# Kernel optimization log

Measured on AMD Instinct MI355X. Metric: run time of the kernel, lower is better.

The kernel has to match this reference:

```python
import jax, jax.numpy as jnp
import numpy as np

# Module / shape constants (match init_kwargs and forward-path constants)
H = 8          # heads
DH = 80        # dim_head
QDIM = 640     # query_dim == inner_dim (context = x, self-attention content branch)
B = 1
NQ = 2048      # query tokens
NS = 2048      # injected style tokens
T = 1.2        # injection_config['T']  (attn_matrix_scale)
GAMMA = 0.3    # injection_config['gamma'] (q_mix)
LAMBDA_MAX = 2.5
TOPK = 128     # style_topk
STYLE_SCALE = 1.0
SCALE = DH ** -0.5


def _split_heads(t, h):
    # 'b n (h d) -> (b h) n d'
    b, n, hd = t.shape
    return t.reshape(b, n, h, hd // h).transpose(0, 2, 1, 3).reshape(b * h, n, hd // h)


def setup_inputs() -> dict:
    key = jax.random.key(0)
    ks = jax.random.split(key, 9)
    x = jax.random.normal(ks[0], (B, NQ, QDIM), jnp.float32)
    Q_c_injected = jax.random.normal(ks[1], (H, NQ, DH), jnp.float32) * 0.5
    K_s_injected = jax.random.normal(ks[2], (H, NS, DH), jnp.float32) * 0.5
    V_s_injected = jax.random.normal(ks[3], (H, NS, DH), jnp.float32) * 0.5
    # Learned params (nn.Linear weights are [out, in]; no bias on q/k/v)
    Wq = jax.random.normal(ks[4], (H * DH, QDIM), jnp.float32) * 0.02
    Wk = jax.random.normal(ks[5], (H * DH, QDIM), jnp.float32) * 0.02
    Wv = jax.random.normal(ks[6], (H * DH, QDIM), jnp.float32) * 0.02
    Wo = jax.random.normal(ks[7], (QDIM, H * DH), jnp.float32) * 0.02
    bo = jnp.zeros((QDIM,), jnp.float32)
    ada_gate = jnp.array([0.2], jnp.float32)
    return {"x": x, "Q_c_injected": Q_c_injected, "K_s_injected": K_s_injected,
            "V_s_injected": V_s_injected, "Wq": Wq, "Wk": Wk, "Wv": Wv,
            "Wo": Wo, "bo": bo, "ada_gate": ada_gate}


def reference(x, Q_c_injected, K_s_injected, V_s_injected, Wq, Wk, Wv, Wo, bo, ada_gate):
    b, n, _ = x.shape
    # Projections, context = x
    q_cs = _split_heads(x @ Wq.T, H)                    # (b h) n d
    k_cs = _split_heads(x @ Wk.T, H)                    # (b h) m d
    v_cs = _split_heads(x @ Wv.T, H)
    Q_c = jnp.tile(Q_c_injected, (b, 1, 1))             # torch.cat([Q_c]*b)
    q = Q_c * GAMMA + q_cs * (1.0 - GAMMA)              # Q_hat_cs
    K_s = jnp.tile(K_s_injected, (b, 1, 1))
    V_s = jnp.tile(V_s_injected, (b, 1, 1))

    style = jnp.einsum('bid,bjd->bij', q, K_s) * (T * SCALE)   # (bh) nq ns
    content = jnp.einsum('bid,bjd->bij', q, k_cs) * SCALE       # (bh) nq nc
    ns = style.shape[-1]
    s4 = style.reshape(b, H, n, ns)
    c4 = content.reshape(b, H, n, -1)

    # Per-head logsumexp gating between style and content branches
    r = jax.scipy.special.logsumexp(s4, axis=-1) - jax.scipy.special.logsumexp(c4, axis=-1)
    r = jnp.clip(r, -20.0, 20.0).mean(axis=1)           # (b, nq)
    lam = 1.0 + (LAMBDA_MAX - 1.0) * jax.nn.sigmoid(r)  # lambda_map
    style = (s4 * lam[:, None, :, None]).reshape(b * H, n, ns)

    # Top-k sparsification of style logits (scatter top-k values onto -inf canvas)
    vals, idx = jax.lax.top_k(style, TOPK)
    neg = jnp.finfo(style.dtype).min
    bi = jnp.arange(b * H)[:, None, None]
    ni = jnp.arange(n)[None, :, None]
    style = jnp.full_like(style, neg).at[bi, ni, idx].set(vals)

    logits = jnp.concatenate([style, content], axis=-1)
    attn = jax.nn.softmax(logits, axis=-1)
    v = jnp.concatenate([V_s * STYLE_SCALE, v_cs], axis=1)      # (bh) (ns+nc) d
    out = jnp.einsum('bij,bjd->bid', attn, v)

    # AdaIN-style modulation
    A = attn.reshape(b, H, n, -1)
    Vh = v.reshape(b, H, -1, DH)
    Qh = q.reshape(b, H, n, DH)
    Vmean = jnp.einsum('bhnm,bhmd->bhnd', A, Vh)
    mu = Qh.mean(axis=2, keepdims=True)
    var = Qh.var(axis=2, keepdims=True)                 # unbiased=False
    Qn = (Qh - mu) / jnp.sqrt(var + 1e-5)
    Vsq = jnp.einsum('bhnm,bhmd->bhnd', A, Vh * Vh)
    Vstd = jnp.sqrt(jnp.clip(Vsq - Vmean ** 2, 1e-5))
    out_mod = (Vstd * Qn + Vmean).reshape(b * H, n, DH)  # use_std_scale path

    g = jnp.tanh(ada_gate[0])                            # use_residual_gate
    out = out + g * (out_mod - out)
    out = out.reshape(b, H, n, DH).transpose(0, 2, 1, 3).reshape(b, n, H * DH)
    return out @ Wo.T + bo                               # to_out (dropout=0)
```

## Files before the change

### kernel.cpp

```cpp
#include <hip/hip_runtime.h>
#include <hip/hip_fp16.h>
#include <math.h>

#define NH 8
#define DH 80
#define NTOK 2048
#define QD 640
#define SCALE_F 0.11180339887498949f
#define TSCALE_F (1.2f * SCALE_F)
#define GAMMA_F 0.3f
#define LMAX_F 2.5f
#define TOPKN 128

typedef __attribute__((ext_vector_type(8))) short bf16x8;
typedef __attribute__((ext_vector_type(4))) float f32x4;
typedef __attribute__((ext_vector_type(4))) unsigned short u16x4;

#define OFF_QB   0u
#define OFF_OB   1310720u
#define OFF_QH   2621440u
#define OFF_QL   3407872u
#define OFF_KCH  4194304u
#define OFF_KSH  4980736u
#define OFF_KSL  5767168u
#define OFF_VCT  6553600u
#define OFF_VCQT 7208960u
#define OFF_VST  7864320u
#define OFF_VSQT 8519680u
#define OFF_OP   9175040u
#define OFF_SP   14417920u
#define OFF_DEN  19660800u
#define OFF_MSZ  19726336u
#define OFF_LSZ  19791872u
#define OFF_MCZ  19857408u
#define OFF_LCZ  19922944u
#define OFF_M    19988480u
#define OFF_LAM  20004864u
#define OFF_THR  20006912u
#define OFF_MU   20023296u
#define OFF_RSTD 20023936u
#define OFF_S16  20024576u

static __device__ __forceinline__ unsigned short f2bf(float f) {
  unsigned u = __float_as_uint(f);
  return (unsigned short)((u + 0x7FFFu + ((u >> 16) & 1u)) >> 16);
}
static __device__ __forceinline__ float bf2f(unsigned short s) {
  return __uint_as_float(((unsigned)s) << 16);
}
static __device__ __forceinline__ unsigned sk16(unsigned u) {
  return (u & 0x8000u) ? (~u & 0xFFFFu) : (u | 0x8000u);
}

__global__ __launch_bounds__(256) void k_projmm(
    const float* __restrict__ x, const float* __restrict__ Wq,
    const float* __restrict__ Wk, const float* __restrict__ Wv,
    const float* __restrict__ Qc, float* __restrict__ qb,
    unsigned short* __restrict__ qh_, unsigned short* __restrict__ ql_,
    unsigned short* __restrict__ kch_,
    unsigned short* __restrict__ vct_, unsigned short* __restrict__ vcqt_)
{
  const float* W = (blockIdx.z == 0) ? Wq : ((blockIdx.z == 1) ? Wk : Wv);
  const int n0 = blockIdx.y * 64, c0 = blockIdx.x * 64;
  const int tid = threadIdx.x;
  const int w = tid >> 6, l = tid & 63;
  const int cc = l & 15, g = l >> 4;

  __shared__ unsigned short sXh[64 * 72];
  __shared__ unsigned short sXl[64 * 72];
  __shared__ unsigned short sWh[64 * 72];
  __shared__ unsigned short sWl[64 * 72];

  f32x4 D[4];
#pragma unroll
  for (int ct = 0; ct < 4; ++ct) D[ct] = (f32x4){0.f, 0.f, 0.f, 0.f};

  for (int k0 = 0; k0 < QD; k0 += 64) {
    __syncthreads();
#pragma unroll
    for (int it = 0; it < 4; ++it) {
      int f = tid + it * 256;
      int row = f >> 4, col4 = f & 15;
      float4 xa = *(const float4*)(x + (size_t)(n0 + row) * QD + k0 + col4 * 4);
      float4 wa = *(const float4*)(W + (size_t)(c0 + row) * QD + k0 + col4 * 4);
      u16x4 xh, xl, wh, wl;
      float xv[4] = {xa.x, xa.y, xa.z, xa.w};
      float wv[4] = {wa.x, wa.y, wa.z, wa.w};
#pragma unroll
      for (int j = 0; j < 4; ++j) {
        unsigned short h1 = f2bf(xv[j]);
        xh[j] = h1; xl[j] = f2bf(xv[j] - bf2f(h1));
        unsigned short h2 = f2bf(wv[j]);
        wh[j] = h2; wl[j] = f2bf(wv[j] - bf2f(h2));
      }
      *(u16x4*)&sXh[row * 72 + col4 * 4] = xh;
      *(u16x4*)&sXl[row * 72 + col4 * 4] = xl;
      *(u16x4*)&sWh[row * 72 + col4 * 4] = wh;
      *(u16x4*)&sWl[row * 72 + col4 * 4] = wl;
    }
    __syncthreads();
    bf16x8 ah[2], al[2];
#pragma unroll
    for (int kc = 0; kc < 2; ++kc) {
      ah[kc] = *(const bf16x8*)&sXh[(w * 16 + cc) * 72 + kc * 32 + g * 8];
      al[kc] = *(const bf16x8*)&sXl[(w * 16 + cc) * 72 + kc * 32 + g * 8];
    }
#pragma unroll
    for (int ct = 0; ct < 4; ++ct) {
#pragma unroll
      for (int kc = 0; kc < 2; ++kc) {
        bf16x8 bh = *(const bf16x8*)&sWh[(ct * 16 + cc) * 72 + kc * 32 + g * 8];
        bf16x8 bl = *(const bf16x8*)&sWl[(ct * 16 + cc) * 72 + kc * 32 + g * 8];
        D[ct] = __builtin_amdgcn_mfma_f32_16x16x32_bf16(ah[kc], bh, D[ct], 0, 0, 0);
        D[ct] = __builtin_amdgcn_mfma_f32_16x16x32_bf16(ah[kc], bl, D[ct], 0, 0, 0);
        D[ct] = __builtin_amdgcn_mfma_f32_16x16x32_bf16(al[kc], bh, D[ct], 0, 0, 0);
      }
    }
  }
#pragma unroll
  for (int ct = 0; ct < 4; ++ct) {
#pragma unroll
    for (int r = 0; r < 4; ++r) {
      int n = n0 + w * 16 + g * 4 + r;
      int ccol = c0 + ct * 16 + cc;
      int h = ccol / DH, d = ccol - h * DH;
      size_t i80 = ((size_t)h * NTOK + n) * 80 + d;
      size_t i96 = ((size_t)h * NTOK + n) * 96 + d;
      float val = D[ct][r];
      if (blockIdx.z == 0) {
        val = GAMMA_F * Qc[i80] + (1.f - GAMMA_F) * val;
        qb[i80] = val;
        unsigned short hs = f2bf(val);
        qh_[i96] = hs;
        ql_[i96] = f2bf(val - bf2f(hs));
      } else if (blockIdx.z == 1) {
        kch_[i96] = f2bf(val);
      } else {
        size_t iT = (((size_t)h * 80 + d) << 11) + n;
        vct_[iT]  = f2bf(val);
        vcqt_[iT] = f2bf(val * val);
      }
    }
  }
}

__global__ __launch_bounds__(256) void k_cvt(
    const float* __restrict__ Ks, const float* __restrict__ Vs,
    unsigned short* __restrict__ Ksh, unsigned short* __restrict__ Ksl,
    unsigned short* __restrict__ VTs, unsigned short* __restrict__ VTqs,
    unsigned short* __restrict__ qh_, unsigned short* __restrict__ ql_,
    unsigned short* __restrict__ kch_)
{
  const int h = blockIdx.y;
  const int n0 = blockIdx.x * 64;
  const int tid = threadIdx.x;
  __shared__ unsigned short sVT[80 * 68];
  __shared__ unsigned short sVQ[80 * 68];

  for (int f = tid; f < 1280; f += 256) {
    int rr = f / 20, dc = f % 20;
    size_t i80 = ((size_t)h * NTOK + n0 + rr) * 80 + dc * 4;
    size_t i96 = ((size_t)h * NTOK + n0 + rr) * 96 + dc * 4;
    float4 kv = *(const float4*)(Ks + i80);
    float kvv[4] = {kv.x, kv.y, kv.z, kv.w};
    u16x4 kh, kl;
#pragma unroll
    for (int j = 0; j < 4; ++j) {
      unsigned short hs = f2bf(kvv[j]);
      kh[j] = hs; kl[j] = f2bf(kvv[j] - bf2f(hs));
    }
    *(u16x4*)(Ksh + i96) = kh;
    *(u16x4*)(Ksl + i96) = kl;
    float4 vv = *(const float4*)(Vs + i80);
    float vvv[4] = {vv.x, vv.y, vv.z, vv.w};
#pragma unroll
    for (int j = 0; j < 4; ++j) {
      int d = dc * 4 + j;
      sVT[d * 68 + rr] = f2bf(vvv[j]);
      sVQ[d * 68 + rr] = f2bf(vvv[j] * vvv[j]);
    }
  }
  for (int f = tid; f < 1024; f += 256) {
    int rr = f >> 4, dcol = 80 + (f & 15);
    size_t i96 = ((size_t)h * NTOK + n0 + rr) * 96 + dcol;
    Ksh[i96] = 0; Ksl[i96] = 0; qh_[i96] = 0; ql_[i96] = 0; kch_[i96] = 0;
  }
  __syncthreads();
  for (int f = tid; f < 640; f += 256) {
    int d = f >> 3, kp8 = f & 7;
    size_t iT = (((size_t)h * 80 + d) << 11) + n0 + kp8 * 8;
    *(bf16x8*)(VTs + iT)  = *(const bf16x8*)&sVT[d * 68 + kp8 * 8];
    *(bf16x8*)(VTqs + iT) = *(const bf16x8*)&sVQ[d * 68 + kp8 * 8];
  }
}

__global__ __launch_bounds__(128) void k_qstats(
    const float* __restrict__ qb, float* __restrict__ mu, float* __restrict__ rstd)
{
  const int h = blockIdx.x / DH, d = blockIdx.x % DH;
  const int tid = threadIdx.x;
  float s = 0.f, s2 = 0.f;
  for (int n = tid; n < NTOK; n += 128) {
    float v = qb[((size_t)h * NTOK + n) * 80 + d];
    s += v; s2 = fmaf(v, v, s2);
  }
#pragma unroll
  for (int off = 32; off; off >>= 1) { s += __shfl_xor(s, off, 64); s2 += __shfl_xor(s2, off, 64); }
  __shared__ float sh[4];
  if ((tid & 63) == 0) { sh[(tid >> 6) * 2] = s; sh[(tid >> 6) * 2 + 1] = s2; }
  __syncthreads();
  if (tid == 0) {
    float S = sh[0] + sh[2], S2 = sh[1] + sh[3];
    float mval = S * (1.f / NTOK);
    float var = S2 * (1.f / NTOK) - mval * mval;
    mu[h * DH + d] = mval;
    rstd[h * DH + d] = rsqrtf(var + 1e-5f);
  }
}

__global__ __launch_bounds__(256) void k_passA(
    const unsigned short* __restrict__ qh_, const unsigned short* __restrict__ ql_,
    const unsigned short* __restrict__ Ksh, const unsigned short* __restrict__ Ksl,
    const unsigned short* __restrict__ kch_,
    unsigned short* __restrict__ S16, float* __restrict__ mSz, float* __restrict__ lSz,
    float* __restrict__ mCz, float* __restrict__ lCz)
{
  const int bid = blockIdx.x;
  const int swz = (bid & 7) * 128 + (bid >> 3);
  const int q0 = (swz & 31) * 64;
  const int h  = (swz >> 5) & 7;
  const int z  = swz >> 8;
  const int tid = threadIdx.x;
  const int w = tid >> 6, l = tid & 63;
  const int c = l & 15, g = l >> 4;

  __shared__ unsigned short sKh[64 * 104];
  __shared__ unsigned short sKl[64 * 104];

  bf16x8 qhf[3], qlf[3];
  {
    const size_t qrow = ((size_t)h * NTOK + q0 + w * 16 + c) * 96;
#pragma unroll
    for (int kc = 0; kc < 3; ++kc) {
      qhf[kc] = *(const bf16x8*)(qh_ + qrow + kc * 32 + g * 8);
      qlf[kc] = *(const bf16x8*)(ql_ + qrow + kc * 32 + g * 8);
    }
  }
  float m[4], lse[4], mc[4], lc[4];
#pragma unroll
  for (int r = 0; r < 4; ++r) { m[r] = -INFINITY; lse[r] = 0.f; mc[r] = -INFINITY; lc[r] = 0.f; }

  for (int t = 0; t < 8; ++t) {
    const size_t kbase = ((size_t)h * NTOK + z * 512 + t * 64) * 96;
    __syncthreads();
    for (int f = tid; f < 768; f += 256) {
      int row = f / 12, ch = f % 12;
      *(bf16x8*)(sKh + row * 104 + ch * 8) = *(const bf16x8*)(Ksh + kbase + row * 96 + ch * 8);
      *(bf16x8*)(sKl + row * 104 + ch * 8) = *(const bf16x8*)(Ksl + kbase + row * 96 + ch * 8);
    }
    __syncthreads();
#pragma unroll
    for (int ct = 0; ct < 4; ++ct) {
      f32x4 D = {0.f, 0.f, 0.f, 0.f};
      const int krow = (ct * 16 + c) * 104 + g * 8;
#pragma unroll
      for (int kc = 0; kc < 3; ++kc) {
        bf16x8 bh = *(const bf16x8*)(sKh + krow + kc * 32);
        D = __builtin_amdgcn_mfma_f32_16x16x32_bf16(qhf[kc], bh, D, 0, 0, 0);
      }
#pragma unroll
      for (int kc = 0; kc < 3; ++kc) {
        bf16x8 bl = *(const bf16x8*)(sKl + krow + kc * 32);
        D = __builtin_amdgcn_mfma_f32_16x16x32_bf16(qhf[kc], bl, D, 0, 0, 0);
      }
#pragma unroll
      for (int kc = 0; kc < 3; ++kc) {
        bf16x8 bh = *(const bf16x8*)(sKh + krow + kc * 32);
        D = __builtin_amdgcn_mfma_f32_16x16x32_bf16(qlf[kc], bh, D, 0, 0, 0);
      }
#pragma unroll
      for (int r = 0; r < 4; ++r) {
        float s = D[r] * TSCALE_F;
        __half hh = __float2half(s);
        S16[((size_t)h * NTOK + q0 + w * 16 + g * 4 + r) * 2048 + z * 512 + t * 64 + ct * 16 + c] =
            __half_as_ushort(hh);
        float mn = fmaxf(m[r], s);
        lse[r] = lse[r] * __expf(m[r] - mn) + __expf(s - mn);
        m[r] = mn;
      }
    }
  }
  for (int t = 0; t < 8; ++t) {
    const size_t kbase = ((size_t)h * NTOK + z * 512 + t * 64) * 96;
    __syncthreads();
    for (int f = tid; f < 768; f += 256) {
      int row = f / 12, ch = f % 12;
      *(bf16x8*)(sKh + row * 104 + ch * 8) = *(const bf16x8*)(kch_ + kbase + row * 96 + ch * 8);
    }
    __syncthreads();
#pragma unroll
    for (int ct = 0; ct < 4; ++ct) {
      f32x4 D = {0.f, 0.f, 0.f, 0.f};
      const int krow = (ct * 16 + c) * 104 + g * 8;
#pragma unroll
      for (int kc = 0; kc < 3; ++kc) {
        bf16x8 bh = *(const bf16x8*)(sKh + krow + kc * 32);
        D = __builtin_amdgcn_mfma_f32_16x16x32_bf16(qhf[kc], bh, D, 0, 0, 0);
      }
#pragma unroll
      for (int r = 0; r < 4; ++r) {
        float s = D[r] * SCALE_F;
        float mn = fmaxf(mc[r], s);
        lc[r] = lc[r] * __expf(mc[r] - mn) + __expf(s - mn);
        mc[r] = mn;
      }
    }
  }
#pragma unroll
  for (int off = 1; off < 16; off <<= 1) {
#pragma unroll
    for (int r = 0; r < 4; ++r) {
      float mo = __shfl_xor(m[r], off, 64), lo = __shfl_xor(lse[r], off, 64);
      float mn = fmaxf(m[r], mo);
      lse[r] = lse[r] * __expf(m[r] - mn) + lo * __expf(mo - mn);
      m[r] = mn;
      float mo2 = __shfl_xor(mc[r], off, 64), lo2 = __shfl_xor(lc[r], off, 64);
      float mn2 = fmaxf(mc[r], mo2);
      lc[r] = lc[r] * __expf(mc[r] - mn2) + lo2 * __expf(mo2 - mn2);
      mc[r] = mn2;
    }
  }
  if (c == 0) {
    size_t base = (size_t)(z * 8 + h) * NTOK + q0 + w * 16 + g * 4;
#pragma unroll
    for (int r = 0; r < 4; ++r) {
      mSz[base + r] = m[r]; lSz[base + r] = lse[r];
      mCz[base + r] = mc[r]; lCz[base + r] = lc[r];
    }
  }
}

__global__ __launch_bounds__(256) void k_gate(
    const float* __restrict__ mSz, const float* __restrict__ lSz,
    const float* __restrict__ mCz, const float* __restrict__ lCz,
    float* __restrict__ M_, float* __restrict__ lam_)
{
  int n = blockIdx.x * 256 + threadIdx.x;
  if (n >= NTOK) return;
  float msf[NH], mcf[NH], sum = 0.f;
#pragma unroll
  for (int h = 0; h < NH; ++h) {
    float mm = -INFINITY, cm = -INFINITY;
#pragma unroll
    for (int zz = 0; zz < 4; ++zz) {
      mm = fmaxf(mm, mSz[(size_t)(zz * 8 + h) * NTOK + n]);
      cm = fmaxf(cm, mCz[(size_t)(zz * 8 + h) * NTOK + n]);
    }
    float ls = 0.f, lcs = 0.f;
#pragma unroll
    for (int zz = 0; zz < 4; ++zz) {
      ls  += lSz[(size_t)(zz * 8 + h) * NTOK + n] * __expf(mSz[(size_t)(zz * 8 + h) * NTOK + n] - mm);
      lcs += lCz[(size_t)(zz * 8 + h) * NTOK + n] * __expf(mCz[(size_t)(zz * 8 + h) * NTOK + n] - cm);
    }
    float lse_s = mm + __logf(ls);
    float lse_c = cm + __logf(lcs);
    msf[h] = mm; mcf[h] = cm;
    sum += fminf(fmaxf(lse_s - lse_c, -20.f), 20.f);
  }
  float lam = 1.f + (LMAX_F - 1.f) * (1.f / (1.f + __expf(-sum * (1.f / NH))));
  lam_[n] = lam;
#pragma unroll
  for (int h = 0; h < NH; ++h)
    M_[h * NTOK + n] = fmaxf(lam * msf[h], mcf[h]);
}

__global__ __launch_bounds__(512) void k_topk(const unsigned short* __restrict__ S16,
                                              unsigned* __restrict__ thr_)
{
  const int h = blockIdx.y;
  const int n = blockIdx.x * 8 + (threadIdx.x >> 6);
  const int l = threadIdx.x & 63;
  const unsigned short* Srow = S16 + ((size_t)h * NTOK + n) * 2048;
  unsigned kv[32];
#pragma unroll
  for (int t = 0; t < 4; ++t) {
    uint4 v = ((const uint4*)Srow)[t * 64 + l];
    unsigned dw[4] = {v.x, v.y, v.z, v.w};
#pragma unroll
    for (int i = 0; i < 8; ++i) {
      unsigned u = (dw[i >> 1] >> ((i & 1) * 16)) & 0xFFFFu;
      kv[t * 8 + i] = sk16(u);
    }
  }
  unsigned klo = 0u, khi = 65536u;
  for (int it = 0; it < 16; ++it) {
    unsigned mid = (klo + khi) >> 1;
    int cnt = 0;
#pragma unroll
    for (int t = 0; t < 32; ++t)
      cnt += __popcll(__ballot(kv[t] >= mid));
    if (cnt == TOPKN) { klo = mid; break; }
    if (cnt > TOPKN) klo = mid; else khi = mid;
    if (khi - klo <= 1u) break;
  }
  if (l == 0) thr_[h * NTOK + n] = klo;
}

__global__ __launch_bounds__(256) void k_passB(
    const unsigned short* __restrict__ qh_, const unsigned short* __restrict__ kch_,
    const unsigned short* __restrict__ VTs, const unsigned short* __restrict__ VTqs,
    const unsigned short* __restrict__ VTc, const unsigned short* __restrict__ VTqc,
    const unsigned short* __restrict__ S16,
    const float* __restrict__ M_, const float* __restrict__ lam_,
    const unsigned* __restrict__ thr_,
    float* __restrict__ oP, float* __restrict__ sP, float* __restrict__ denP)
{
  const int bid = blockIdx.x;
  const int swz = (bid & 7) * 128 + (bid >> 3);
  const int q0 = (swz & 31) * 64;
  const int h  = (swz >> 5) & 7;
  const int z  = swz >> 8;
  const int tid = threadIdx.x;
  const int w = tid >> 6, l = tid & 63;
  const int c = l & 15, g = l >> 4;

  __shared__ char arena[45568];
  unsigned short* S_lds   = (unsigned short*)arena;
  unsigned short* kch_lds = (unsigned short*)arena;
  unsigned short* P_lds   = (unsigned short*)(arena + 13312);
  unsigned short* vT      = (unsigned short*)(arena + 22528);
  unsigned short* vqT     = (unsigned short*)(arena + 34048);
  __shared__ float Mr[64], lamr[64], den_l[64];
  __shared__ unsigned thrr[64];

  if (tid < 64) {
    int n = q0 + tid;
    Mr[tid] = M_[h * NTOK + n];
    lamr[tid] = lam_[n];
    thrr[tid] = thr_[h * NTOK + n];
    den_l[tid] = 0.f;
  }
  bf16x8 qhf[3];
  {
    const size_t qrow = ((size_t)h * NTOK + q0 + w * 16 + c) * 96;
#pragma unroll
    for (int kc = 0; kc < 3; ++kc)
      qhf[kc] = *(const bf16x8*)(qh_ + qrow + kc * 32 + g * 8);
  }
  __syncthreads();
  const float myLam = lamr[w * 16 + c], myM = Mr[w * 16 + c];
  const unsigned myThr = thrr[w * 16 + c];
  float myM4[4];
#pragma unroll
  for (int r = 0; r < 4; ++r) myM4[r] = Mr[w * 16 + g * 4 + r];

  f32x4 oacc[5], sacc[5];
#pragma unroll
  for (int dt = 0; dt < 5; ++dt) { oacc[dt] = (f32x4){0.f,0.f,0.f,0.f}; sacc[dt] = (f32x4){0.f,0.f,0.f,0.f}; }
  float denS = 0.f, denC[4] = {0.f, 0.f, 0.f, 0.f};

  for (int t = 0; t < 8; ++t) {
    const int k0 = z * 512 + t * 64;
    __syncthreads();
    for (int f = tid; f < 512; f += 256) {
      int row = f >> 3, ch = f & 7;
      *(uint4*)&S_lds[row * 72 + ch * 8] =
          *(const uint4*)(S16 + ((size_t)h * NTOK + q0 + row) * 2048 + k0 + ch * 8);
    }
    for (int f = tid; f < 640; f += 256) {
      int d = f >> 3, kp8 = f & 7;
      size_t iT = (((size_t)h * 80 + d) << 11) + k0 + kp8 * 8;
      *(bf16x8*)&vT[d * 72 + kp8 * 8]  = *(const bf16x8*)(VTs + iT);
      *(bf16x8*)&vqT[d * 72 + kp8 * 8] = *(const bf16x8*)(VTqs + iT);
    }
    __syncthreads();
    bf16x8 pa[2];
#pragma unroll
    for (int kc = 0; kc < 2; ++kc) {
      uint4 sv = *(const uint4*)&S_lds[(w * 16 + c) * 72 + kc * 32 + g * 8];
      unsigned dw[4] = {sv.x, sv.y, sv.z, sv.w};
      bf16x8 pk;
#pragma unroll
      for (int i = 0; i < 8; ++i) {
        unsigned u = (dw[i >> 1] >> ((i & 1) * 16)) & 0xFFFFu;
        float s = __half2float(__ushort_as_half((unsigned short)u));
        float wv = (sk16(u) >= myThr) ? __expf(myLam * s - myM) : 0.f;
        denS += wv;
        pk[i] = (short)f2bf(wv);
      }
      pa[kc] = pk;
    }
#pragma unroll
    for (int dt = 0; dt < 5; ++dt) {
#pragma unroll
      for (int kc = 0; kc < 2; ++kc) {
        bf16x8 bv  = *(const bf16x8*)&vT[(dt * 16 + c) * 72 + kc * 32 + g * 8];
        bf16x8 bvq = *(const bf16x8*)&vqT[(dt * 16 + c) * 72 + kc * 32 + g * 8];
        oacc[dt] = __builtin_amdgcn_mfma_f32_16x16x32_bf16(pa[kc], bv, oacc[dt], 0, 0, 0);
        sacc[dt] = __builtin_amdgcn_mfma_f32_16x16x32_bf16(pa[kc], bvq, sacc[dt], 0, 0, 0);
      }
    }
  }
  for (int t = 0; t < 8; ++t) {
    const int k0 = z * 512 + t * 64;
    __syncthreads();
    for (int f = tid; f < 768; f += 256) {
      int row = f / 12, ch = f % 12;
      *(bf16x8*)(kch_lds + row * 104 + ch * 8) =
          *(const bf16x8*)(kch_ + ((size_t)h * NTOK + k0 + row) * 96 + ch * 8);
    }
    for (int f = tid; f < 640; f += 256) {
      int d = f >> 3, kp8 = f & 7;
      size_t iT = (((size_t)h * 80 + d) << 11) + k0 + kp8 * 8;
      *(bf16x8*)&vT[d * 72 + kp8 * 8]  = *(const bf16x8*)(VTc + iT);
      *(bf16x8*)&vqT[d * 72 + kp8 * 8] = *(const bf16x8*)(VTqc + iT);
    }
    __syncthreads();
#pragma unroll
    for (int ct = 0; ct < 4; ++ct) {
      f32x4 D = {0.f, 0.f, 0.f, 0.f};
      const int krow = (ct * 16 + c) * 104 + g * 8;
#pragma unroll
      for (int kc = 0; kc < 3; ++kc) {
        bf16x8 bh = *(const bf16x8*)(kch_lds + krow + kc * 32);
        D = __builtin_amdgcn_mfma_f32_16x16x32_bf16(qhf[kc], bh, D, 0, 0, 0);
      }
#pragma unroll
      for (int r = 0; r < 4; ++r) {
        float s = D[r] * SCALE_F;
        float wv = __expf(s - myM4[r]);
        denC[r] += wv;
        P_lds[w * 1152 + (g * 4 + r) * 72 + ct * 16 + c] = f2bf(wv);
      }
    }
    bf16x8 pa0 = *(const bf16x8*)(P_lds + w * 1152 + c * 72 + g * 8);
    bf16x8 pa1 = *(const bf16x8*)(P_lds + w * 1152 + c * 72 + 32 + g * 8);
#pragma unroll
    for (int dt = 0; dt < 5; ++dt) {
      bf16x8 bv0  = *(const bf16x8*)&vT[(dt * 16 + c) * 72 + g * 8];
      bf16x8 bvq0 = *(const bf16x8*)&vqT[(dt * 16 + c) * 72 + g * 8];
      bf16x8 bv1  = *(const bf16x8*)&vT[(dt * 16 + c) * 72 + 32 + g * 8];
      bf16x8 bvq1 = *(const bf16x8*)&vqT[(dt * 16 + c) * 72 + 32 + g * 8];
      oacc[dt] = __builtin_amdgcn_mfma_f32_16x16x32_bf16(pa0, bv0, oacc[dt], 0, 0, 0);
      sacc[dt] = __builtin_amdgcn_mfma_f32_16x16x32_bf16(pa0, bvq0, sacc[dt], 0, 0, 0);
      oacc[dt] = __builtin_amdgcn_mfma_f32_16x16x32_bf16(pa1, bv1, oacc[dt], 0, 0, 0);
      sacc[dt] = __builtin_amdgcn_mfma_f32_16x16x32_bf16(pa1, bvq1, sacc[dt], 0, 0, 0);
    }
  }
  denS += __shfl_xor(denS, 16, 64);
  denS += __shfl_xor(denS, 32, 64);
#pragma unroll
  for (int off = 1; off < 16; off <<= 1)
#pragma unroll
    for (int r = 0; r < 4; ++r) denC[r] += __shfl_xor(denC[r], off, 64);
  if (l < 16) atomicAdd(&den_l[w * 16 + l], denS);
  if (c == 0) {
#pragma unroll
    for (int r = 0; r < 4; ++r) atomicAdd(&den_l[w * 16 + g * 4 + r], denC[r]);
  }
  __syncthreads();
  const size_t base = (size_t)(z * 8 + h) * NTOK + q0 + w * 16;
#pragma unroll
  for (int dt = 0; dt < 5; ++dt)
#pragma unroll
    for (int r = 0; r < 4; ++r) {
      size_t o = (base + g * 4 + r) * 80 + dt * 16 + c;
      oP[o] = oacc[dt][r];
      sP[o] = sacc[dt][r];
    }
  if (tid < 64) denP[(size_t)(z * 8 + h) * NTOK + q0 + tid] = den_l[tid];
}

__global__ __launch_bounds__(256) void k_fin(
    const float* __restrict__ oP, const float* __restrict__ sP,
    const float* __restrict__ denP, const float* __restrict__ qb,
    const float* __restrict__ mu, const float* __restrict__ rstd,
    const float* __restrict__ gate, float* __restrict__ Ob)
{
  int idx = blockIdx.x * 256 + threadIdx.x;
  int h = idx / (NTOK * 80);
  int rem = idx - h * (NTOK * 80);
  int n = rem / 80, d = rem - n * 80;
  float den = 0.f, o = 0.f, sq = 0.f;
#pragma unroll
  for (int zz = 0; zz < 4; ++zz) {
    den += denP[(size_t)(zz * 8 + h) * NTOK + n];
    size_t p = ((size_t)(zz * 8 + h) * NTOK + n) * 80 + d;
    o += oP[p];
    sq += sP[p];
  }
  o /= den;
  sq /= den;
  float vstd = sqrtf(fmaxf(sq - o * o, 1e-5f));
  float g = tanhf(gate[0]);
  float qn = (qb[((size_t)h * NTOK + n) * 80 + d] - mu[h * DH + d]) * rstd[h * DH + d];
  Ob[(size_t)n * QD + h * DH + d] = fmaf(g * vstd, qn, o);
}

__global__ __launch_bounds__(256) void k_finalmm(
    const float* __restrict__ A, const float* __restrict__ W,
    const float* __restrict__ bias, float* __restrict__ out)
{
  const int n0 = blockIdx.y * 64, c0 = blockIdx.x * 64;
  const int tid = threadIdx.x;
  const int w = tid >> 6, l = tid & 63;
  const int cc = l & 15, g = l >> 4;

  __shared__ unsigned short sXh[64 * 72];
  __shared__ unsigned short sXl[64 * 72];
  __shared__ unsigned short sWh[64 * 72];
  __shared__ unsigned short sWl[64 * 72];

  f32x4 D[4];
#pragma unroll
  for (int ct = 0; ct < 4; ++ct) D[ct] = (f32x4){0.f, 0.f, 0.f, 0.f};

  for (int k0 = 0; k0 < QD; k0 += 64) {
    __syncthreads();
#pragma unroll
    for (int it = 0; it < 4; ++it) {
      int f = tid + it * 256;
      int row = f >> 4, col4 = f & 15;
      float4 xa = *(const float4*)(A + (size_t)(n0 + row) * QD + k0 + col4 * 4);
      float4 wa = *(const float4*)(W + (size_t)(c0 + row) * QD + k0 + col4 * 4);
      u16x4 xh, xl, wh, wl;
      float xv[4] = {xa.x, xa.y, xa.z, xa.w};
      float wv[4] = {wa.x, wa.y, wa.z, wa.w};
#pragma unroll
      for (int j = 0; j < 4; ++j) {
        unsigned short h1 = f2bf(xv[j]);
        xh[j] = h1; xl[j] = f2bf(xv[j] - bf2f(h1));
        unsigned short h2 = f2bf(wv[j]);
        wh[j] = h2; wl[j] = f2bf(wv[j] - bf2f(h2));
      }
      *(u16x4*)&sXh[row * 72 + col4 * 4] = xh;
      *(u16x4*)&sXl[row * 72 + col4 * 4] = xl;
      *(u16x4*)&sWh[row * 72 + col4 * 4] = wh;
      *(u16x4*)&sWl[row * 72 + col4 * 4] = wl;
    }
    __syncthreads();
    bf16x8 ah[2], al[2];
#pragma unroll
    for (int kc = 0; kc < 2; ++kc) {
      ah[kc] = *(const bf16x8*)&sXh[(w * 16 + cc) * 72 + kc * 32 + g * 8];
      al[kc] = *(const bf16x8*)&sXl[(w * 16 + cc) * 72 + kc * 32 + g * 8];
    }
#pragma unroll
    for (int ct = 0; ct < 4; ++ct) {
#pragma unroll
      for (int kc = 0; kc < 2; ++kc) {
        bf16x8 bh = *(const bf16x8*)&sWh[(ct * 16 + cc) * 72 + kc * 32 + g * 8];
        bf16x8 bl = *(const bf16x8*)&sWl[(ct * 16 + cc) * 72 + kc * 32 + g * 8];
        D[ct] = __builtin_amdgcn_mfma_f32_16x16x32_bf16(ah[kc], bh, D[ct], 0, 0, 0);
        D[ct] = __builtin_amdgcn_mfma_f32_16x16x32_bf16(ah[kc], bl, D[ct], 0, 0, 0);
        D[ct] = __builtin_amdgcn_mfma_f32_16x16x32_bf16(al[kc], bh, D[ct], 0, 0, 0);
      }
    }
  }
#pragma unroll
  for (int ct = 0; ct < 4; ++ct) {
#pragma unroll
    for (int r = 0; r < 4; ++r) {
      int n = n0 + w * 16 + g * 4 + r;
      int ccol = c0 + ct * 16 + cc;
      out[(size_t)n * QD + ccol] = D[ct][r] + bias[ccol];
    }
  }
}

extern "C" void kernel_launch(void* const* d_in, const int* in_sizes, int n_in,
                              void* d_out, int out_size, void* d_ws, size_t ws_size,
                              hipStream_t stream) {
  const float* x    = (const float*)d_in[0];
  const float* Qc   = (const float*)d_in[1];
  const float* Ks   = (const float*)d_in[2];
  const float* Vs   = (const float*)d_in[3];
  const float* Wq   = (const float*)d_in[4];
  const float* Wk   = (const float*)d_in[5];
  const float* Wv   = (const float*)d_in[6];
  const float* Wo   = (const float*)d_in[7];
  const float* bo   = (const float*)d_in[8];
  const float* gate = (const float*)d_in[9];
  float* out = (float*)d_out;
  float* w = (float*)d_ws;

  float* qb   = w + OFF_QB;
  float* Ob   = w + OFF_OB;
  unsigned short* qh_  = (unsigned short*)(w + OFF_QH);
  unsigned short* ql_  = (unsigned short*)(w + OFF_QL);
  unsigned short* kch_ = (unsigned short*)(w + OFF_KCH);
  unsigned short* Ksh  = (unsigned short*)(w + OFF_KSH);
  unsigned short* Ksl  = (unsigned short*)(w + OFF_KSL);
  unsigned short* VTc  = (unsigned short*)(w + OFF_VCT);
  unsigned short* VTqc = (unsigned short*)(w + OFF_VCQT);
  unsigned short* VTs  = (unsigned short*)(w + OFF_VST);
  unsigned short* VTqs = (unsigned short*)(w + OFF_VSQT);
  float* oP   = w + OFF_OP;
  float* sP   = w + OFF_SP;
  float* denP = w + OFF_DEN;
  float* mSz  = w + OFF_MSZ;
  float* lSz  = w + OFF_LSZ;
  float* mCz  = w + OFF_MCZ;
  float* lCz  = w + OFF_LCZ;
  float* M_   = w + OFF_M;
  float* lam_ = w + OFF_LAM;
  unsigned* thr_ = (unsigned*)(w + OFF_THR);
  float* mu   = w + OFF_MU;
  float* rstd = w + OFF_RSTD;
  unsigned short* S16 = (unsigned short*)(w + OFF_S16);

  k_projmm<<<dim3(10, 32, 3), 256, 0, stream>>>(x, Wq, Wk, Wv, Qc, qb, qh_, ql_, kch_, VTc, VTqc);
  k_cvt<<<dim3(32, 8), 256, 0, stream>>>(Ks, Vs, Ksh, Ksl, VTs, VTqs, qh_, ql_, kch_);
  k_qstats<<<dim3(640), 128, 0, stream>>>(qb, mu, rstd);
  k_passA<<<dim3(1024), 256, 0, stream>>>(qh_, ql_, Ksh, Ksl, kch_, S16, mSz, lSz, mCz, lCz);
  k_gate<<<dim3(8), 256, 0, stream>>>(mSz, lSz, mCz, lCz, M_, lam_);
  k_topk<<<dim3(256, 8), 512, 0, stream>>>(S16, thr_);
  k_passB<<<dim3(1024), 256, 0, stream>>>(qh_, kch_, VTs, VTqs, VTc, VTqc, S16, M_, lam_, thr_, oP, sP, denP);
  k_fin<<<dim3(5120), 256, 0, stream>>>(oP, sP, denP, qb, mu, rstd, gate, Ob);
  k_finalmm<<<dim3(10, 32), 256, 0, stream>>>(Ob, Wo, bo, out);
}
```

Measured before the change: 304.2 us.

## Store content logits in passA and reuse them in passB instead of recomputing

passA now writes the scaled content logits as fp16 to a new workspace buffer, and passB reads them instead of reloading K_c and recomputing QK^T with MFMA. passB is also restructured into a single 16-iteration loop over style and content tiles. In that loop the logits go straight from global memory into registers, the V loads are issued before the barrier, and the per-row denominator is reduced with shuffles instead of LDS atomics. This removes recomputation and LDS staging, but adds about 64 MB of fp16 writes and reads and rounds the content logits to fp16.

Result: faster. 267.5 us (-12.1%).

```diff
diff --git a/kernel.cpp b/kernel.cpp
--- a/kernel.cpp
+++ b/kernel.cpp
@@ -40,6 +40,7 @@
 #define OFF_MU   20023296u
 #define OFF_RSTD 20023936u
 #define OFF_S16  20024576u
+#define OFF_SC16 36801792u
 
 static __device__ __forceinline__ unsigned short f2bf(float f) {
   unsigned u = __float_as_uint(f);
@@ -222,7 +223,8 @@
     const unsigned short* __restrict__ qh_, const unsigned short* __restrict__ ql_,
     const unsigned short* __restrict__ Ksh, const unsigned short* __restrict__ Ksl,
     const unsigned short* __restrict__ kch_,
-    unsigned short* __restrict__ S16, float* __restrict__ mSz, float* __restrict__ lSz,
+    unsigned short* __restrict__ S16, unsigned short* __restrict__ Sc16,
+    float* __restrict__ mSz, float* __restrict__ lSz,
     float* __restrict__ mCz, float* __restrict__ lCz)
 {
   const int bid = blockIdx.x;
@@ -281,9 +283,8 @@
 #pragma unroll
       for (int r = 0; r < 4; ++r) {
         float s = D[r] * TSCALE_F;
-        __half hh = __float2half(s);
         S16[((size_t)h * NTOK + q0 + w * 16 + g * 4 + r) * 2048 + z * 512 + t * 64 + ct * 16 + c] =
-            __half_as_ushort(hh);
+            __half_as_ushort(__float2half(s));
         float mn = fmaxf(m[r], s);
         lse[r] = lse[r] * __expf(m[r] - mn) + __expf(s - mn);
         m[r] = mn;
@@ -310,6 +311,8 @@
 #pragma unroll
       for (int r = 0; r < 4; ++r) {
         float s = D[r] * SCALE_F;
+        Sc16[((size_t)h * NTOK + q0 + w * 16 + g * 4 + r) * 2048 + z * 512 + t * 64 + ct * 16 + c] =
+            __half_as_ushort(__float2half(s));
         float mn = fmaxf(mc[r], s);
         lc[r] = lc[r] * __expf(mc[r] - mn) + __expf(s - mn);
         mc[r] = mn;
@@ -407,10 +410,9 @@
 }
 
 __global__ __launch_bounds__(256) void k_passB(
-    const unsigned short* __restrict__ qh_, const unsigned short* __restrict__ kch_,
     const unsigned short* __restrict__ VTs, const unsigned short* __restrict__ VTqs,
     const unsigned short* __restrict__ VTc, const unsigned short* __restrict__ VTqc,
-    const unsigned short* __restrict__ S16,
+    const unsigned short* __restrict__ S16, const unsigned short* __restrict__ Sc16,
     const float* __restrict__ M_, const float* __restrict__ lam_,
     const unsigned* __restrict__ thr_,
     float* __restrict__ oP, float* __restrict__ sP, float* __restrict__ denP)
@@ -424,117 +426,73 @@
   const int w = tid >> 6, l = tid & 63;
   const int c = l & 15, g = l >> 4;
 
-  __shared__ char arena[45568];
-  unsigned short* S_lds   = (unsigned short*)arena;
-  unsigned short* kch_lds = (unsigned short*)arena;
-  unsigned short* P_lds   = (unsigned short*)(arena + 13312);
-  unsigned short* vT      = (unsigned short*)(arena + 22528);
-  unsigned short* vqT     = (unsigned short*)(arena + 34048);
-  __shared__ float Mr[64], lamr[64], den_l[64];
-  __shared__ unsigned thrr[64];
-
-  if (tid < 64) {
-    int n = q0 + tid;
-    Mr[tid] = M_[h * NTOK + n];
-    lamr[tid] = lam_[n];
-    thrr[tid] = thr_[h * NTOK + n];
-    den_l[tid] = 0.f;
-  }
-  bf16x8 qhf[3];
-  {
-    const size_t qrow = ((size_t)h * NTOK + q0 + w * 16 + c) * 96;
-#pragma unroll
-    for (int kc = 0; kc < 3; ++kc)
-      qhf[kc] = *(const bf16x8*)(qh_ + qrow + kc * 32 + g * 8);
-  }
-  __syncthreads();
-  const float myLam = lamr[w * 16 + c], myM = Mr[w * 16 + c];
-  const unsigned myThr = thrr[w * 16 + c];
-  float myM4[4];
-#pragma unroll
-  for (int r = 0; r < 4; ++r) myM4[r] = Mr[w * 16 + g * 4 + r];
+  __shared__ unsigned short vT[80 * 72];
+  __shared__ unsigned short vqT[80 * 72];
+
+  const int myrow = w * 16 + c;
+  const float myM = M_[h * NTOK + q0 + myrow];
+  const float myLam = lam_[q0 + myrow];
+  const unsigned myThr = thr_[h * NTOK + q0 + myrow];
+
+  const size_t srow = ((size_t)h * NTOK + q0 + myrow) * 2048 + g * 8;
+  const int d0 = tid >> 3, kp8 = tid & 7;
+  const size_t vr0 = (((size_t)h * 80 + d0) << 11) + kp8 * 8;
+  const size_t vr1 = (((size_t)h * 80 + d0 + 32) << 11) + kp8 * 8;
+  const size_t vr2 = (((size_t)h * 80 + d0 + 64) << 11) + kp8 * 8;
+  const bool third = (tid < 128);
 
   f32x4 oacc[5], sacc[5];
 #pragma unroll
   for (int dt = 0; dt < 5; ++dt) { oacc[dt] = (f32x4){0.f,0.f,0.f,0.f}; sacc[dt] = (f32x4){0.f,0.f,0.f,0.f}; }
-  float denS = 0.f, denC[4] = {0.f, 0.f, 0.f, 0.f};
-
-  for (int t = 0; t < 8; ++t) {
-    const int k0 = z * 512 + t * 64;
-    __syncthreads();
-    for (int f = tid; f < 512; f += 256) {
-      int row = f >> 3, ch = f & 7;
-      *(uint4*)&S_lds[row * 72 + ch * 8] =
-          *(const uint4*)(S16 + ((size_t)h * NTOK + q0 + row) * 2048 + k0 + ch * 8);
-    }
-    for (int f = tid; f < 640; f += 256) {
-      int d = f >> 3, kp8 = f & 7;
-      size_t iT = (((size_t)h * 80 + d) << 11) + k0 + kp8 * 8;
-      *(bf16x8*)&vT[d * 72 + kp8 * 8]  = *(const bf16x8*)(VTs + iT);
-      *(bf16x8*)&vqT[d * 72 + kp8 * 8] = *(const bf16x8*)(VTqs + iT);
-    }
-    __syncthreads();
-    bf16x8 pa[2];
-#pragma unroll
-    for (int kc = 0; kc < 2; ++kc) {
-      uint4 sv = *(const uint4*)&S_lds[(w * 16 + c) * 72 + kc * 32 + g * 8];
-      unsigned dw[4] = {sv.x, sv.y, sv.z, sv.w};
-      bf16x8 pk;
+  float den = 0.f;
+
+  for (int t = 0; t < 16; ++t) {
+    const bool style = (t < 8);
+    const int k0 = z * 512 + (t & 7) * 64;
+    const unsigned short* Sp = style ? S16 : Sc16;
+    const unsigned short* Vp = style ? VTs : VTc;
+    const unsigned short* Vq = style ? VTqs : VTqc;
+    uint4 s0 = *(const uint4*)(Sp + srow + k0);
+    uint4 s1 = *(const uint4*)(Sp + srow + k0 + 32);
+    bf16x8 v0 = *(const bf16x8*)(Vp + vr0 + k0);
+    bf16x8 v1 = *(const bf16x8*)(Vp + vr1 + k0);
+    bf16x8 u0 = *(const bf16x8*)(Vq + vr0 + k0);
+    bf16x8 u1 = *(const bf16x8*)(Vq + vr1 + k0);
+    bf16x8 v2, u2;
+    if (third) {
+      v2 = *(const bf16x8*)(Vp + vr2 + k0);
+      u2 = *(const bf16x8*)(Vq + vr2 + k0);
+    }
+    __syncthreads();
+    *(bf16x8*)&vT[d0 * 72 + kp8 * 8] = v0;
+    *(bf16x8*)&vqT[d0 * 72 + kp8 * 8] = u0;
+    *(bf16x8*)&vT[(d0 + 32) * 72 + kp8 * 8] = v1;
+    *(bf16x8*)&vqT[(d0 + 32) * 72 + kp8 * 8] = u1;
+    if (third) {
+      *(bf16x8*)&vT[(d0 + 64) * 72 + kp8 * 8] = v2;
+      *(bf16x8*)&vqT[(d0 + 64) * 72 + kp8 * 8] = u2;
+    }
+    __syncthreads();
+    bf16x8 pa0, pa1;
+    {
+      unsigned dw0[4] = {s0.x, s0.y, s0.z, s0.w};
+      unsigned dw1[4] = {s1.x, s1.y, s1.z, s1.w};
 #pragma unroll
       for (int i = 0; i < 8; ++i) {
-        unsigned u = (dw[i >> 1] >> ((i & 1) * 16)) & 0xFFFFu;
-        float s = __half2float(__ushort_as_half((unsigned short)u));
-        float wv = (sk16(u) >= myThr) ? __expf(myLam * s - myM) : 0.f;
-        denS += wv;
-        pk[i] = (short)f2bf(wv);
-      }
-      pa[kc] = pk;
-    }
-#pragma unroll
-    for (int dt = 0; dt < 5; ++dt) {
-#pragma unroll
-      for (int kc = 0; kc < 2; ++kc) {
-        bf16x8 bv  = *(const bf16x8*)&vT[(dt * 16 + c) * 72 + kc * 32 + g * 8];
-        bf16x8 bvq = *(const bf16x8*)&vqT[(dt * 16 + c) * 72 + kc * 32 + g * 8];
-        oacc[dt] = __builtin_amdgcn_mfma_f32_16x16x32_bf16(pa[kc], bv, oacc[dt], 0, 0, 0);
-        sacc[dt] = __builtin_amdgcn_mfma_f32_16x16x32_bf16(pa[kc], bvq, sacc[dt], 0, 0, 0);
-      }
-    }
-  }
-  for (int t = 0; t < 8; ++t) {
-    const int k0 = z * 512 + t * 64;
-    __syncthreads();
-    for (int f = tid; f < 768; f += 256) {
-      int row = f / 12, ch = f % 12;
-      *(bf16x8*)(kch_lds + row * 104 + ch * 8) =
-          *(const bf16x8*)(kch_ + ((size_t)h * NTOK + k0 + row) * 96 + ch * 8);
-    }
-    for (int f = tid; f < 640; f += 256) {
-      int d = f >> 3, kp8 = f & 7;
-      size_t iT = (((size_t)h * 80 + d) << 11) + k0 + kp8 * 8;
-      *(bf16x8*)&vT[d * 72 + kp8 * 8]  = *(const bf16x8*)(VTc + iT);
-      *(bf16x8*)&vqT[d * 72 + kp8 * 8] = *(const bf16x8*)(VTqc + iT);
-    }
-    __syncthreads();
-#pragma unroll
-    for (int ct = 0; ct < 4; ++ct) {
-      f32x4 D = {0.f, 0.f, 0.f, 0.f};
-      const int krow = (ct * 16 + c) * 104 + g * 8;
-#pragma unroll
-      for (int kc = 0; kc < 3; ++kc) {
-        bf16x8 bh = *(const bf16x8*)(kch_lds + krow + kc * 32);
-        D = __builtin_amdgcn_mfma_f32_16x16x32_bf16(qhf[kc], bh, D, 0, 0, 0);
-      }
-#pragma unroll
-      for (int r = 0; r < 4; ++r) {
-        float s = D[r] * SCALE_F;
-        float wv = __expf(s - myM4[r]);
-        denC[r] += wv;
-        P_lds[w * 1152 + (g * 4 + r) * 72 + ct * 16 + c] = f2bf(wv);
-      }
-    }
-    bf16x8 pa0 = *(const bf16x8*)(P_lds + w * 1152 + c * 72 + g * 8);
-    bf16x8 pa1 = *(const bf16x8*)(P_lds + w * 1152 + c * 72 + 32 + g * 8);
+        unsigned ua = (dw0[i >> 1] >> ((i & 1) * 16)) & 0xFFFFu;
+        float sa = __half2float(__ushort_as_half((unsigned short)ua));
+        float wa = style ? ((sk16(ua) >= myThr) ? __expf(myLam * sa - myM) : 0.f)
+                         : __expf(sa - myM);
+        den += wa;
+        pa0[i] = (short)f2bf(wa);
+        unsigned ub = (dw1[i >> 1] >> ((i & 1) * 16)) & 0xFFFFu;
+        float sb = __half2float(__ushort_as_half((unsigned short)ub));
+        float wb = style ? ((sk16(ub) >= myThr) ? __expf(myLam * sb - myM) : 0.f)
+                         : __expf(sb - myM);
+        den += wb;
+        pa1[i] = (short)f2bf(wb);
+      }
+    }
 #pragma unroll
     for (int dt = 0; dt < 5; ++dt) {
       bf16x8 bv0  = *(const bf16x8*)&vT[(dt * 16 + c) * 72 + g * 8];
@@ -547,18 +505,9 @@
       sacc[dt] = __builtin_amdgcn_mfma_f32_16x16x32_bf16(pa1, bvq1, sacc[dt], 0, 0, 0);
     }
   }
-  denS += __shfl_xor(denS, 16, 64);
-  denS += __shfl_xor(denS, 32, 64);
-#pragma unroll
-  for (int off = 1; off < 16; off <<= 1)
-#pragma unroll
-    for (int r = 0; r < 4; ++r) denC[r] += __shfl_xor(denC[r], off, 64);
-  if (l < 16) atomicAdd(&den_l[w * 16 + l], denS);
-  if (c == 0) {
-#pragma unroll
-    for (int r = 0; r < 4; ++r) atomicAdd(&den_l[w * 16 + g * 4 + r], denC[r]);
-  }
-  __syncthreads();
+  den += __shfl_xor(den, 16, 64);
+  den += __shfl_xor(den, 32, 64);
+  if (g == 0) denP[(size_t)(z * 8 + h) * NTOK + q0 + myrow] = den;
   const size_t base = (size_t)(z * 8 + h) * NTOK + q0 + w * 16;
 #pragma unroll
   for (int dt = 0; dt < 5; ++dt)
@@ -568,7 +517,6 @@
       oP[o] = oacc[dt][r];
       sP[o] = sacc[dt][r];
     }
-  if (tid < 64) denP[(size_t)(z * 8 + h) * NTOK + q0 + tid] = den_l[tid];
 }
 
 __global__ __launch_bounds__(256) void k_fin(
@@ -707,15 +655,16 @@
   unsigned* thr_ = (unsigned*)(w + OFF_THR);
   float* mu   = w + OFF_MU;
   float* rstd = w + OFF_RSTD;
-  unsigned short* S16 = (unsigned short*)(w + OFF_S16);
+  unsigned short* S16  = (unsigned short*)(w + OFF_S16);
+  unsigned short* Sc16 = (unsigned short*)(w + OFF_SC16);
 
   k_projmm<<<dim3(10, 32, 3), 256, 0, stream>>>(x, Wq, Wk, Wv, Qc, qb, qh_, ql_, kch_, VTc, VTqc);
   k_cvt<<<dim3(32, 8), 256, 0, stream>>>(Ks, Vs, Ksh, Ksl, VTs, VTqs, qh_, ql_, kch_);
   k_qstats<<<dim3(640), 128, 0, stream>>>(qb, mu, rstd);
-  k_passA<<<dim3(1024), 256, 0, stream>>>(qh_, ql_, Ksh, Ksl, kch_, S16, mSz, lSz, mCz, lCz);
+  k_passA<<<dim3(1024), 256, 0, stream>>>(qh_, ql_, Ksh, Ksl, kch_, S16, Sc16, mSz, lSz, mCz, lCz);
   k_gate<<<dim3(8), 256, 0, stream>>>(mSz, lSz, mCz, lCz, M_, lam_);
   k_topk<<<dim3(256, 8), 512, 0, stream>>>(S16, thr_);
-  k_passB<<<dim3(1024), 256, 0, stream>>>(qh_, kch_, VTs, VTqs, VTc, VTqc, S16, M_, lam_, thr_, oP, sP, denP);
+  k_passB<<<dim3(1024), 256, 0, stream>>>(VTs, VTqs, VTc, VTqc, S16, Sc16, M_, lam_, thr_, oP, sP, denP);
   k_fin<<<dim3(5120), 256, 0, stream>>>(oP, sP, denP, qb, mu, rstd, gate, Ob);
   k_finalmm<<<dim3(10, 32), 256, 0, stream>>>(Ob, Wo, bo, out);
 }
```
